# Performance work log

Measured on AMD Instinct MI355X. Metric: run time of the kernel, lower is better.

Reference implementation:

```python
import jax, jax.numpy as jnp
import numpy as np

NN_SIZE = 16  # nn_size from __init__


def _knn_idx(points_ref, k):
    """Brute-force KNN of points_ref against itself (replaces faiss_knn).
    Returns (B, N, k) neighbor indices, self point excluded."""
    sq = jnp.sum(points_ref * points_ref, axis=-1)  # (B, N)
    # squared pairwise distances (B, N, N)
    d2 = sq[:, :, None] + sq[:, None, :] - 2.0 * jnp.einsum(
        'bnd,bmd->bnm', points_ref, points_ref)
    _, idx = jax.lax.top_k(-d2, k + 1)  # nearest first; idx[...,0] is self
    return idx[:, :, 1:]


def _edge_lengths(pts, knn_idx):
    """Gather neighbor coords and compute edge lengths (B, N, K)."""
    group = jax.vmap(lambda p, i: p[i])(pts, knn_idx)  # (B, N, K, D)
    return jnp.linalg.norm(group - pts[:, :, None, :], axis=-1)


def setup_inputs() -> dict:
    key = jax.random.key(0)
    k1, k2 = jax.random.split(key)
    B, N, D = 4, 8192, 3
    points_ref = jax.random.normal(k1, (B, N, D), dtype=jnp.float32)
    # pred points: perturbed ref so the loss is non-degenerate
    points = points_ref + 0.01 * jax.random.normal(k2, (B, N, D), dtype=jnp.float32)
    return {"points_ref": points_ref, "points": points}


def reference(points_ref, points):
    # faiss KNN is non-differentiable -> stop_gradient on the index search
    knn_idx = _knn_idx(jax.lax.stop_gradient(points_ref), NN_SIZE)  # (B,N,K)
    dist_ref = _edge_lengths(points_ref, knn_idx)  # (B, N, K)
    dist = _edge_lengths(points, knn_idx)          # (B, N, K)
    # metric = torch.nn.L1Loss() (mean reduction)
    return jnp.mean(jnp.abs(dist_ref - dist))
```

## Files before the change

kernel.cpp:

```cpp
#include <hip/hip_runtime.h>
#include <math.h>

#define BATCH 4
#define NPTS  8192
#define KNN   16
#define KK    17
#define NQ    (BATCH*NPTS)
#define JMASK 0x1FFFu
#define EMASK 0xFFFFE000u
#define TOTAL_EDGES (BATCH*NPTS*KNN)

#define GC    32
#define GLO   (-4.5f)
#define GINV  (32.0f/9.0f)
#define NCELL (GC*GC*GC)

#define QPB   64
#define BLOCK 512
#define NWAVE 8
#define SLICE (NPTS/NWAVE)
#define GRIDQ (NQ/QPB)
#define WIN   64

__device__ __forceinline__ int cell_coord(float x) {
    int c = (int)floorf((x - GLO) * GINV);
    return min(GC - 1, max(0, c));
}
__device__ __forceinline__ unsigned spread5(unsigned v) {
    v &= 31u;
    v = (v | (v << 8)) & 0x100Fu;
    v = (v | (v << 4)) & 0x10C3u;
    v = (v | (v << 2)) & 0x1249u;
    return v;
}
__device__ __forceinline__ unsigned morton_id(float x, float y, float z) {
    return spread5((unsigned)cell_coord(x)) | (spread5((unsigned)cell_coord(y)) << 1)
         | (spread5((unsigned)cell_coord(z)) << 2);
}
__device__ __forceinline__ unsigned mkkey(const float4 p, float xi, float yi,
                                          float zi, float sqi, unsigned j) {
    const float e  = fmaf(p.x, xi, fmaf(p.y, yi, p.z * zi)) + p.w;
    const float d2 = e + sqi;
    return (__float_as_uint(d2) & EMASK) | j;
}
__device__ __forceinline__ void ins17(unsigned (&a)[KK], unsigned key) {
    #pragma unroll
    for (int k = KK - 1; k >= 1; --k) a[k] = min(a[k], max(a[k - 1], key));
    a[0] = min(a[0], key);
}

__global__ void pel_hist(const float* __restrict__ pref, unsigned* __restrict__ hist,
                         float* __restrict__ acc, unsigned* __restrict__ bcnt) {
    const int idx = blockIdx.x * 256 + threadIdx.x;
    if (idx == 0) { acc[0] = 0.0f; bcnt[0] = 0u; }
    const int b = idx >> 13;
    const unsigned mid = morton_id(pref[3*idx], pref[3*idx+1], pref[3*idx+2]);
    atomicAdd(&hist[b * NCELL + mid], 1u);
}
__global__ __launch_bounds__(1024)
void pel_scan(const unsigned* __restrict__ hist, unsigned* __restrict__ off) {
    __shared__ unsigned s[1024];
    const unsigned* h = hist + blockIdx.x * NCELL;
    unsigned*       o = off  + blockIdx.x * NCELL;
    const int t = threadIdx.x;
    unsigned v[32], tot = 0;
    #pragma unroll
    for (int k = 0; k < 32; ++k) { v[k] = h[t * 32 + k]; tot += v[k]; }
    s[t] = tot;
    __syncthreads();
    for (int d = 1; d < 1024; d <<= 1) {
        const unsigned add = (t >= d) ? s[t - d] : 0u;
        __syncthreads();
        s[t] += add;
        __syncthreads();
    }
    unsigned run = s[t] - tot;
    #pragma unroll
    for (int k = 0; k < 32; ++k) { o[t * 32 + k] = run; run += v[k]; }
}
__global__ void pel_scatter(const float* __restrict__ pref, const float* __restrict__ pts,
                            unsigned* __restrict__ off,
                            float4* __restrict__ p4r, float4* __restrict__ p4p) {
    const int idx = blockIdx.x * 256 + threadIdx.x;
    const int b = idx >> 13;
    const float x = pref[3*idx], y = pref[3*idx+1], z = pref[3*idx+2];
    const unsigned mid = morton_id(x, y, z);
    const unsigned pos = atomicAdd(&off[b * NCELL + mid], 1u);
    p4r[b * NPTS + pos] = make_float4(-2.f*x, -2.f*y, -2.f*z, fmaf(x, x, fmaf(y, y, z*z)));
    const float px = pts[3*idx], py = pts[3*idx+1], pz = pts[3*idx+2];
    p4p[b * NPTS + pos] = make_float4(-2.f*px, -2.f*py, -2.f*pz,
                                      fmaf(px, px, fmaf(py, py, pz*pz)));
}

__global__ __launch_bounds__(BLOCK, 4)
void pel_query(const float4* __restrict__ P4r, const float4* __restrict__ P4p,
               float* __restrict__ acc_ws, unsigned* __restrict__ bcnt,
               float* __restrict__ out)
{
    __shared__ unsigned s_pool[KK][BLOCK];
    __shared__ float s_part[NWAVE];

    const int t = threadIdx.x;
    const int l = t & 63, w = t >> 6;
    const int q = blockIdx.x * QPB + l;
    const int b = q >> 13;
    const int i = q & (NPTS - 1);

    const float4* __restrict__ Pq = P4r + b * NPTS;
    const float4* __restrict__ Pp = P4p + b * NPTS;

    const float4 self = Pq[i];
    const float xi = -0.5f * self.x, yi = -0.5f * self.y, zi = -0.5f * self.z;
    const float sqi = self.w;

    unsigned t17[KK];
    #pragma unroll
    for (int k = 0; k < KK; ++k) t17[k] = 0xFFFFFFFFu;
    const int w0 = min(max(i - WIN / 2, 0), NPTS - WIN);
    for (int u = 0; u < WIN; ++u) {
        const unsigned key = mkkey(Pq[w0 + u], xi, yi, zi, sqi, (unsigned)(w0 + u));
        if (key <= t17[KK - 1]) ins17(t17, key);
    }
    unsigned tauL = t17[KK - 1];

    unsigned c17[KK];
    #pragma unroll
    for (int k = 0; k < KK; ++k) c17[k] = 0xFFFFFFFFu;
    const int jb = w << 10;
    float4 p0 = Pq[jb], p1 = Pq[jb + 1], p2 = Pq[jb + 2], p3 = Pq[jb + 3];
    for (int j = 0; j < SLICE; j += 4) {
        const int jn = jb + ((j + 4) & (SLICE - 1));
        const float4 n0 = Pq[jn],     n1 = Pq[jn + 1];
        const float4 n2 = Pq[jn + 2], n3 = Pq[jn + 3];
        unsigned key;
        key = mkkey(p0, xi, yi, zi, sqi, (unsigned)(jb + j));
        if (key <= tauL) { ins17(c17, key); tauL = min(tauL, c17[KK - 1]); }
        key = mkkey(p1, xi, yi, zi, sqi, (unsigned)(jb + j + 1));
        if (key <= tauL) { ins17(c17, key); tauL = min(tauL, c17[KK - 1]); }
        key = mkkey(p2, xi, yi, zi, sqi, (unsigned)(jb + j + 2));
        if (key <= tauL) { ins17(c17, key); tauL = min(tauL, c17[KK - 1]); }
        key = mkkey(p3, xi, yi, zi, sqi, (unsigned)(jb + j + 3));
        if (key <= tauL) { ins17(c17, key); tauL = min(tauL, c17[KK - 1]); }
        p0 = n0; p1 = n1; p2 = n2; p3 = n3;
    }

    #pragma unroll
    for (int k = 0; k < KK; ++k) s_pool[k][t] = c17[k];
    __syncthreads();
    #pragma unroll 1
    for (int d = 1; d < NWAVE; ++d) {
        const int t2 = (((w + d) & (NWAVE - 1)) << 6) | l;
        #pragma unroll 1
        for (int k = 0; k < KK; ++k) {
            const unsigned vk = s_pool[k][t2];
            if (vk >= c17[KK - 1]) break;
            ins17(c17, vk);
        }
    }

    const float4 selfp = Pp[i];
    const float pxi = -0.5f * selfp.x, pyi = -0.5f * selfp.y, pzi = -0.5f * selfp.z;
    float accv = 0.0f;
    for (int r = w; r < KK; r += NWAVE) {
        const int j = (int)(c17[r] & JMASK);
        const float4 pr = Pq[j];
        const float er  = fmaf(pr.x, xi, fmaf(pr.y, yi, pr.z * zi)) + pr.w;
        const float d2r = fmaxf(er + sqi, 0.0f);
        const float4 pp = Pp[j];
        const float ep  = fmaf(pp.x, pxi, fmaf(pp.y, pyi, pp.z * pzi)) + pp.w;
        const float d2p = fmaxf(ep + selfp.w, 0.0f);
        accv += fabsf(sqrtf(d2r) - sqrtf(d2p));
    }

    #pragma unroll
    for (int o = 32; o > 0; o >>= 1) accv += __shfl_down(accv, o, 64);
    if (l == 0) s_part[w] = accv;
    __syncthreads();
    if (t == 0) {
        float s = 0.0f;
        #pragma unroll
        for (int w2 = 0; w2 < NWAVE; ++w2) s += s_part[w2];
        atomicAdd(acc_ws, s);
        __threadfence();
        const unsigned old = atomicAdd(bcnt, 1u);
        if (old == GRIDQ - 1) {
            __threadfence();
            const float total = atomicAdd(acc_ws, 0.0f);
            out[0] = total * (1.0f / (float)TOTAL_EDGES);
        }
    }
}

extern "C" void kernel_launch(void* const* d_in, const int* in_sizes, int n_in,
                              void* d_out, int out_size, void* d_ws, size_t ws_size,
                              hipStream_t stream) {
    const float* pref = (const float*)d_in[0];
    const float* pts  = (const float*)d_in[1];
    float4*   P4r  = (float4*)d_ws;
    float4*   P4p  = P4r + NQ;
    unsigned* hist = (unsigned*)d_ws;
    unsigned* off  = (unsigned*)((char*)d_ws + 1048576);
    float*    acc  = (float*)((char*)d_ws + 1581056);
    unsigned* bcnt = (unsigned*)(acc + 1);
    float*    out  = (float*)d_out;

    hipMemsetAsync(hist, 0, BATCH * NCELL * sizeof(unsigned), stream);
    pel_hist   <<<NQ / 256, 256, 0, stream>>>(pref, hist, acc, bcnt);
    pel_scan   <<<BATCH, 1024, 0, stream>>>(hist, off);
    pel_scatter<<<NQ / 256, 256, 0, stream>>>(pref, pts, off, P4r, P4p);
    pel_query  <<<GRIDQ, BLOCK, 0, stream>>>(P4r, P4p, acc, bcnt, out);
}
```

Baseline: 261.9 us.

## Buffer candidate keys in per-thread LDS lists and compact them in batches

The scan phase no longer runs a divergent 17-wide sorted insert for each passing candidate. Each thread now appends every key to a per-thread LDS list, advancing the count only when the key passes the threshold. When the list grows past a threshold it is compacted to the best 17 and the threshold is tightened. The merge phase then walks all eight waves' unsorted lists, including the thread's own, with a guarded insert. The change also deepens load prefetch to two groups and uses readfirstlane so the point loads are wave-uniform. The 51 KB LDS list forces launch bounds down to 2 blocks, which lowers occupancy and adds an LDS store for every candidate.

```diff
diff --git a/kernel.cpp b/kernel.cpp
--- a/kernel.cpp
+++ b/kernel.cpp
@@ -21,6 +21,8 @@
 #define SLICE (NPTS/NWAVE)
 #define GRIDQ (NQ/QPB)
 #define WIN   64
+#define LCAP  25
+#define LTH   21
 
 __device__ __forceinline__ int cell_coord(float x) {
     int c = (int)floorf((x - GLO) * GINV);
@@ -92,12 +94,13 @@
                                       fmaf(px, px, fmaf(py, py, pz*pz)));
 }
 
-__global__ __launch_bounds__(BLOCK, 4)
+__global__ __launch_bounds__(BLOCK, 2)
 void pel_query(const float4* __restrict__ P4r, const float4* __restrict__ P4p,
                float* __restrict__ acc_ws, unsigned* __restrict__ bcnt,
                float* __restrict__ out)
 {
-    __shared__ unsigned s_pool[KK][BLOCK];
+    __shared__ unsigned s_list[BLOCK * LCAP];
+    __shared__ int s_cnt[BLOCK];
     __shared__ float s_part[NWAVE];
 
     const int t = threadIdx.x;
@@ -123,38 +126,54 @@
     }
     unsigned tauL = t17[KK - 1];
 
+    unsigned* myl = &s_list[t * LCAP];
+    int cnt = 0;
+    const float4* __restrict__ PqU =
+        P4r + __builtin_amdgcn_readfirstlane(b) * NPTS;
+    const int jb = __builtin_amdgcn_readfirstlane(w) << 10;
+    float4 a0 = PqU[jb + 0], a1 = PqU[jb + 1], a2 = PqU[jb + 2], a3 = PqU[jb + 3];
+    float4 b0 = PqU[jb + 4], b1 = PqU[jb + 5], b2 = PqU[jb + 6], b3 = PqU[jb + 7];
+    for (int j = 0; j < SLICE; j += 4) {
+        const int jn = jb + ((j + 8) & (SLICE - 1));
+        const float4 n0 = PqU[jn],     n1 = PqU[jn + 1];
+        const float4 n2 = PqU[jn + 2], n3 = PqU[jn + 3];
+        unsigned key;
+        key = mkkey(a0, xi, yi, zi, sqi, (unsigned)(jb + j));
+        myl[cnt] = key; cnt += (key <= tauL) ? 1 : 0;
+        key = mkkey(a1, xi, yi, zi, sqi, (unsigned)(jb + j + 1));
+        myl[cnt] = key; cnt += (key <= tauL) ? 1 : 0;
+        key = mkkey(a2, xi, yi, zi, sqi, (unsigned)(jb + j + 2));
+        myl[cnt] = key; cnt += (key <= tauL) ? 1 : 0;
+        key = mkkey(a3, xi, yi, zi, sqi, (unsigned)(jb + j + 3));
+        myl[cnt] = key; cnt += (key <= tauL) ? 1 : 0;
+        if (cnt > LTH) {
+            unsigned a[KK];
+            #pragma unroll
+            for (int k = 0; k < KK; ++k) a[k] = 0xFFFFFFFFu;
+            #pragma unroll 1
+            for (int n = 0; n < cnt; ++n) ins17(a, myl[n]);
+            #pragma unroll
+            for (int k = 0; k < KK; ++k) myl[k] = a[k];
+            cnt = KK; tauL = a[KK - 1];
+        }
+        a0 = b0; a1 = b1; a2 = b2; a3 = b3;
+        b0 = n0; b1 = n1; b2 = n2; b3 = n3;
+    }
+    s_cnt[t] = cnt;
+    __syncthreads();
+
     unsigned c17[KK];
     #pragma unroll
     for (int k = 0; k < KK; ++k) c17[k] = 0xFFFFFFFFu;
-    const int jb = w << 10;
-    float4 p0 = Pq[jb], p1 = Pq[jb + 1], p2 = Pq[jb + 2], p3 = Pq[jb + 3];
-    for (int j = 0; j < SLICE; j += 4) {
-        const int jn = jb + ((j + 4) & (SLICE - 1));
-        const float4 n0 = Pq[jn],     n1 = Pq[jn + 1];
-        const float4 n2 = Pq[jn + 2], n3 = Pq[jn + 3];
-        unsigned key;
-        key = mkkey(p0, xi, yi, zi, sqi, (unsigned)(jb + j));
-        if (key <= tauL) { ins17(c17, key); tauL = min(tauL, c17[KK - 1]); }
-        key = mkkey(p1, xi, yi, zi, sqi, (unsigned)(jb + j + 1));
-        if (key <= tauL) { ins17(c17, key); tauL = min(tauL, c17[KK - 1]); }
-        key = mkkey(p2, xi, yi, zi, sqi, (unsigned)(jb + j + 2));
-        if (key <= tauL) { ins17(c17, key); tauL = min(tauL, c17[KK - 1]); }
-        key = mkkey(p3, xi, yi, zi, sqi, (unsigned)(jb + j + 3));
-        if (key <= tauL) { ins17(c17, key); tauL = min(tauL, c17[KK - 1]); }
-        p0 = n0; p1 = n1; p2 = n2; p3 = n3;
-    }
-
-    #pragma unroll
-    for (int k = 0; k < KK; ++k) s_pool[k][t] = c17[k];
-    __syncthreads();
     #pragma unroll 1
-    for (int d = 1; d < NWAVE; ++d) {
-        const int t2 = (((w + d) & (NWAVE - 1)) << 6) | l;
+    for (int d = 0; d < NWAVE; ++d) {
+        const int ts = (((w + d) & (NWAVE - 1)) << 6) | l;
+        const unsigned* sl = &s_list[ts * LCAP];
+        const int cn = s_cnt[ts];
         #pragma unroll 1
-        for (int k = 0; k < KK; ++k) {
-            const unsigned vk = s_pool[k][t2];
-            if (vk >= c17[KK - 1]) break;
-            ins17(c17, vk);
+        for (int n = 0; n < cn; ++n) {
+            const unsigned vk = sl[n];
+            if (vk <= c17[KK - 1]) ins17(c17, vk);
         }
     }
 
```

New measurement: 582.2 us. 2.22x slower.

## Split each query's candidate scan over 16 slices and share window threshold

Applied to the files above, without the earlier changes.

Each block now handles 32 queries instead of 64, and each query's scan is split across 16 point slices of 512 rather than 8 of 1024. This doubles the grid and shortens each thread's serial scan. The initial pruning threshold comes from a 128-point window, computed once per query by the first 32 threads and shared through LDS, instead of being recomputed redundantly by every wave. Prefetch depth in the scan loop also grows to two groups of four points. In exchange, the other waves sit idle during the window phase, and the cross-slice merge needs 15 rounds instead of 7.

```diff
diff --git a/kernel.cpp b/kernel.cpp
--- a/kernel.cpp
+++ b/kernel.cpp
@@ -15,12 +15,12 @@
 #define GINV  (32.0f/9.0f)
 #define NCELL (GC*GC*GC)
 
-#define QPB   64
+#define QPB   32
 #define BLOCK 512
-#define NWAVE 8
-#define SLICE (NPTS/NWAVE)
+#define NSLC  16
+#define SLICE (NPTS/NSLC)
 #define GRIDQ (NQ/QPB)
-#define WIN   64
+#define WIN   128
 
 __device__ __forceinline__ int cell_coord(float x) {
     int c = (int)floorf((x - GLO) * GINV);
@@ -98,10 +98,11 @@
                float* __restrict__ out)
 {
     __shared__ unsigned s_pool[KK][BLOCK];
-    __shared__ float s_part[NWAVE];
+    __shared__ unsigned s_tau0[QPB];
+    __shared__ float s_part[BLOCK / 64];
 
     const int t = threadIdx.x;
-    const int l = t & 63, w = t >> 6;
+    const int l = t & (QPB - 1), w = t >> 5;
     const int q = blockIdx.x * QPB + l;
     const int b = q >> 13;
     const int i = q & (NPTS - 1);
@@ -113,43 +114,49 @@
     const float xi = -0.5f * self.x, yi = -0.5f * self.y, zi = -0.5f * self.z;
     const float sqi = self.w;
 
-    unsigned t17[KK];
-    #pragma unroll
-    for (int k = 0; k < KK; ++k) t17[k] = 0xFFFFFFFFu;
-    const int w0 = min(max(i - WIN / 2, 0), NPTS - WIN);
-    for (int u = 0; u < WIN; ++u) {
-        const unsigned key = mkkey(Pq[w0 + u], xi, yi, zi, sqi, (unsigned)(w0 + u));
-        if (key <= t17[KK - 1]) ins17(t17, key);
-    }
-    unsigned tauL = t17[KK - 1];
-
+    if (t < QPB) {
+        unsigned t17[KK];
+        #pragma unroll
+        for (int k = 0; k < KK; ++k) t17[k] = 0xFFFFFFFFu;
+        const int w0 = min(max(i - WIN / 2, 0), NPTS - WIN);
+        for (int u = 0; u < WIN; ++u) {
+            const unsigned key = mkkey(Pq[w0 + u], xi, yi, zi, sqi, (unsigned)(w0 + u));
+            if (key <= t17[KK - 1]) ins17(t17, key);
+        }
+        s_tau0[t] = t17[KK - 1];
+    }
+    __syncthreads();
+
+    unsigned tauL = s_tau0[l];
     unsigned c17[KK];
     #pragma unroll
     for (int k = 0; k < KK; ++k) c17[k] = 0xFFFFFFFFu;
-    const int jb = w << 10;
-    float4 p0 = Pq[jb], p1 = Pq[jb + 1], p2 = Pq[jb + 2], p3 = Pq[jb + 3];
+    const int jb = w << 9;
+    float4 a0 = Pq[jb + 0], a1 = Pq[jb + 1], a2 = Pq[jb + 2], a3 = Pq[jb + 3];
+    float4 b0 = Pq[jb + 4], b1 = Pq[jb + 5], b2 = Pq[jb + 6], b3 = Pq[jb + 7];
     for (int j = 0; j < SLICE; j += 4) {
-        const int jn = jb + ((j + 4) & (SLICE - 1));
+        const int jn = jb + ((j + 8) & (SLICE - 1));
         const float4 n0 = Pq[jn],     n1 = Pq[jn + 1];
         const float4 n2 = Pq[jn + 2], n3 = Pq[jn + 3];
         unsigned key;
-        key = mkkey(p0, xi, yi, zi, sqi, (unsigned)(jb + j));
-        if (key <= tauL) { ins17(c17, key); tauL = min(tauL, c17[KK - 1]); }
-        key = mkkey(p1, xi, yi, zi, sqi, (unsigned)(jb + j + 1));
-        if (key <= tauL) { ins17(c17, key); tauL = min(tauL, c17[KK - 1]); }
-        key = mkkey(p2, xi, yi, zi, sqi, (unsigned)(jb + j + 2));
-        if (key <= tauL) { ins17(c17, key); tauL = min(tauL, c17[KK - 1]); }
-        key = mkkey(p3, xi, yi, zi, sqi, (unsigned)(jb + j + 3));
-        if (key <= tauL) { ins17(c17, key); tauL = min(tauL, c17[KK - 1]); }
-        p0 = n0; p1 = n1; p2 = n2; p3 = n3;
+        key = mkkey(a0, xi, yi, zi, sqi, (unsigned)(jb + j));
+        if (key <= tauL) { ins17(c17, key); tauL = min(tauL, c17[KK - 1]); }
+        key = mkkey(a1, xi, yi, zi, sqi, (unsigned)(jb + j + 1));
+        if (key <= tauL) { ins17(c17, key); tauL = min(tauL, c17[KK - 1]); }
+        key = mkkey(a2, xi, yi, zi, sqi, (unsigned)(jb + j + 2));
+        if (key <= tauL) { ins17(c17, key); tauL = min(tauL, c17[KK - 1]); }
+        key = mkkey(a3, xi, yi, zi, sqi, (unsigned)(jb + j + 3));
+        if (key <= tauL) { ins17(c17, key); tauL = min(tauL, c17[KK - 1]); }
+        a0 = b0; a1 = b1; a2 = b2; a3 = b3;
+        b0 = n0; b1 = n1; b2 = n2; b3 = n3;
     }
 
     #pragma unroll
     for (int k = 0; k < KK; ++k) s_pool[k][t] = c17[k];
     __syncthreads();
     #pragma unroll 1
-    for (int d = 1; d < NWAVE; ++d) {
-        const int t2 = (((w + d) & (NWAVE - 1)) << 6) | l;
+    for (int d = 1; d < NSLC; ++d) {
+        const int t2 = ((((w + d) & (NSLC - 1)) << 5) | l);
         #pragma unroll 1
         for (int k = 0; k < KK; ++k) {
             const unsigned vk = s_pool[k][t2];
@@ -161,7 +168,7 @@
     const float4 selfp = Pp[i];
     const float pxi = -0.5f * selfp.x, pyi = -0.5f * selfp.y, pzi = -0.5f * selfp.z;
     float accv = 0.0f;
-    for (int r = w; r < KK; r += NWAVE) {
+    for (int r = w; r < KK; r += NSLC) {
         const int j = (int)(c17[r] & JMASK);
         const float4 pr = Pq[j];
         const float er  = fmaf(pr.x, xi, fmaf(pr.y, yi, pr.z * zi)) + pr.w;
@@ -174,12 +181,12 @@
 
     #pragma unroll
     for (int o = 32; o > 0; o >>= 1) accv += __shfl_down(accv, o, 64);
-    if (l == 0) s_part[w] = accv;
+    if ((t & 63) == 0) s_part[t >> 6] = accv;
     __syncthreads();
     if (t == 0) {
         float s = 0.0f;
         #pragma unroll
-        for (int w2 = 0; w2 < NWAVE; ++w2) s += s_part[w2];
+        for (int w2 = 0; w2 < BLOCK / 64; ++w2) s += s_part[w2];
         atomicAdd(acc_ws, s);
         __threadfence();
         const unsigned old = atomicAdd(bcnt, 1u);
```

After: 330.4 us. 26.2% more time.
